# Performance work log

Hardware: AMD Instinct MI355X
Metric: run time of the kernel (lower is better)

The kernel has to match this reference:

```python
import jax, jax.numpy as jnp
import numpy as np

B, H, L, D = 2, 16, 2048, 64
EPS = 1e-6  # guard for all-zero causal rows after ReLU feature map


def setup_inputs() -> dict:
    key = jax.random.key(0)
    k1, k2, k3, k4, k5 = jax.random.split(key, 5)
    return {
        "query_states": jax.random.normal(k1, (B, H, L, D), dtype=jnp.float32),
        "key_states": jax.random.normal(k2, (B, H, L, D), dtype=jnp.float32),
        "value_states": jax.random.normal(k3, (B, H, L, D), dtype=jnp.float32),
        # LinearFeatureMap params: nn.Parameter(torch.rand(H, D, D)) -> uniform[0,1)
        "fm_query": jax.random.uniform(k4, (H, D, D), dtype=jnp.float32),
        "fm_key": jax.random.uniform(k5, (H, D, D), dtype=jnp.float32),
    }


def _feature_map(states, w):
    # states: [B,H,L,D]; w: [H,D,E]. Matches einsum('blhd,hde->blhe') after transposes.
    return jax.nn.relu(jnp.einsum('bhld,hde->bhle', states, w))


def reference(query_states, key_states, value_states, fm_query, fm_key):
    q = _feature_map(query_states, fm_query)   # [B,H,L,E]
    k = _feature_map(key_states, fm_key)       # [B,H,L,E]
    # quadratic (non-softmax) causal attention
    a = jnp.einsum('bhme,bhne->bhmn', q, k)    # [B,H,L,L]
    causal = jnp.tril(jnp.ones((L, L), dtype=bool))
    a = jnp.where(causal, a, 0.0)
    a = a / (jnp.sum(a, axis=-1, keepdims=True) + EPS)
    return jnp.einsum('bhmn,bhnd->bhmd', a, value_states)
```

## Files before the change

kernel.cpp:

```cpp
#include <hip/hip_runtime.h>
#include <hip/hip_bf16.h>

#define BH_  32
#define H_   16
#define L_   2048
#define D_   64
#define NC_  32
#define STR  72

typedef _Float16 half8  __attribute__((ext_vector_type(8)));
typedef float    floatx4 __attribute__((ext_vector_type(4)));

#define MFMA(a, b, c) __builtin_amdgcn_mfma_f32_16x16x32_f16((a), (b), (c), 0, 0, 0)

__device__ __forceinline__ half8 ldfrag(const _Float16* p, int row0, int k0) {
    const int lane = threadIdx.x & 63;
    const _Float16* q = p + (row0 + (lane & 15)) * STR + k0 + ((lane >> 4) << 3);
    return *(const half8*)q;
}

__global__ __launch_bounds__(256, 2)
void ka_chunksum(const float* __restrict__ K, const float* __restrict__ V,
                 const float* __restrict__ Wk,
                 float* __restrict__ Scs, float* __restrict__ zc) {
    __shared__ _Float16 sKin[64 * STR];
    __shared__ _Float16 sWT [64 * STR];
    __shared__ _Float16 sKT [64 * STR];
    __shared__ _Float16 sVT [64 * STR];

    const int c = blockIdx.x, bh = blockIdx.y, h = bh & (H_ - 1);
    const int tid = threadIdx.x, lane = tid & 63, w = tid >> 6;
    const int quad = lane >> 4, cl = lane & 15;

    const float* Kg = K + ((size_t)bh * L_ + c * 64) * D_;
    const float* Vg = V + ((size_t)bh * L_ + c * 64) * D_;
    const float* Wg = Wk + (size_t)h * 4096;

    for (int i = 0; i < 16; ++i) {
        int flat = i * 256 + tid;
        int r = flat >> 6, e = flat & 63;
        sKin[r * STR + e] = (_Float16)Kg[flat];
        sWT [e * STR + r] = (_Float16)Wg[flat];
        sVT [e * STR + r] = (_Float16)Vg[flat];
    }
    __syncthreads();

    half8 a0 = ldfrag(sKin, w * 16, 0), a1 = ldfrag(sKin, w * 16, 32);
    for (int et = 0; et < 4; ++et) {
        floatx4 acc = {0.f, 0.f, 0.f, 0.f};
        acc = MFMA(a0, ldfrag(sWT, et * 16, 0),  acc);
        acc = MFMA(a1, ldfrag(sWT, et * 16, 32), acc);
        #pragma unroll
        for (int r = 0; r < 4; ++r) {
            float v = acc[r] > 0.f ? acc[r] : 0.f;
            sKT[(et * 16 + cl) * STR + (w * 16 + quad * 4 + r)] = (_Float16)v;
        }
    }
    __syncthreads();

    if (tid < 64) {
        float s = 0.f;
        for (int n = 0; n < 64; ++n) s += (float)sKT[tid * STR + n];
        zc[((size_t)bh * NC_ + c) * 64 + tid] = s;
    }

    float* So = Scs + ((size_t)bh * NC_ + c) * 4096;
    half8 t0 = ldfrag(sKT, w * 16, 0), t1 = ldfrag(sKT, w * 16, 32);
    for (int et = 0; et < 4; ++et) {
        floatx4 acc = {0.f, 0.f, 0.f, 0.f};
        acc = MFMA(t0, ldfrag(sVT, et * 16, 0),  acc);
        acc = MFMA(t1, ldfrag(sVT, et * 16, 32), acc);
        #pragma unroll
        for (int r = 0; r < 4; ++r)
            So[(w * 16 + quad * 4 + r) * 64 + et * 16 + cl] = acc[r];
    }
}

__global__ __launch_bounds__(64)
void kp_prefix(float* __restrict__ Scs, float* __restrict__ zc) {
    const int bid = blockIdx.x, t = threadIdx.x;
    if (bid < BH_ * 64) {
        const int bh = bid >> 6, d = bid & 63;
        size_t base = (size_t)bh * NC_ * 4096 + (size_t)d * 64 + t;
        float run = 0.f;
        #pragma unroll
        for (int c = 0; c < NC_; ++c) {
            float v = Scs[base + (size_t)c * 4096];
            Scs[base + (size_t)c * 4096] = run;
            run += v;
        }
    } else {
        const int bh = bid - BH_ * 64;
        size_t base = (size_t)bh * NC_ * 64 + t;
        float run = 0.f;
        #pragma unroll
        for (int c = 0; c < NC_; ++c) {
            float v = zc[base + c * 64];
            zc[base + c * 64] = run;
            run += v;
        }
    }
}

__global__ __launch_bounds__(256, 2)
void kb_attn(const float* __restrict__ Q, const float* __restrict__ K,
             const float* __restrict__ V, const float* __restrict__ Wq,
             const float* __restrict__ Wk, const float* __restrict__ Sst,
             const float* __restrict__ zs, float* __restrict__ Out) {
    __shared__ _Float16 sQh[64 * STR];
    __shared__ _Float16 sQl[64 * STR];
    __shared__ _Float16 sWh[64 * STR];
    __shared__ _Float16 sWl[64 * STR];
    __shared__ _Float16 sVT[64 * STR];
    __shared__ _Float16 sST[64 * STR];
    __shared__ _Float16 sKB[64 * STR];
    __shared__ float sZ[64];
    __shared__ float sInv[64];

    const int c = blockIdx.x, bh = blockIdx.y, h = bh & (H_ - 1);
    const int tid = threadIdx.x, lane = tid & 63, w = tid >> 6;
    const int quad = lane >> 4, cl = lane & 15;

    const float* Qg = Q + ((size_t)bh * L_ + c * 64) * D_;
    const float* Kg = K + ((size_t)bh * L_ + c * 64) * D_;
    const float* Vg = V + ((size_t)bh * L_ + c * 64) * D_;
    const float* Wqg = Wq + (size_t)h * 4096;
    const float* Wkg = Wk + (size_t)h * 4096;
    const float* Sg = Sst + ((size_t)bh * NC_ + c) * 4096;
    const float* Zg = zs + ((size_t)bh * NC_ + c) * 64;

    for (int i = 0; i < 16; ++i) {
        int flat = i * 256 + tid;
        int r = flat >> 6, e = flat & 63;
        float q = Qg[flat];
        _Float16 qh = (_Float16)q;
        sQh[r * STR + e] = qh;
        sQl[r * STR + e] = (_Float16)(q - (float)qh);
        float wv = Wqg[flat];
        _Float16 wh = (_Float16)wv;
        sWh[e * STR + r] = wh;
        sWl[e * STR + r] = (_Float16)(wv - (float)wh);
        sKB[r * STR + e] = (_Float16)Kg[flat];
        sVT[e * STR + r] = (_Float16)Vg[flat];
        sST[e * STR + r] = (_Float16)Sg[flat];
    }
    if (tid < 64) sZ[tid] = Zg[tid];
    __syncthreads();

    half8 aqh0 = ldfrag(sQh, w * 16, 0), aqh1 = ldfrag(sQh, w * 16, 32);
    half8 aql0 = ldfrag(sQl, w * 16, 0), aql1 = ldfrag(sQl, w * 16, 32);
    float dq[4] = {0.f, 0.f, 0.f, 0.f};
    for (int et = 0; et < 4; ++et) {
        half8 bh0 = ldfrag(sWh, et * 16, 0), bh1 = ldfrag(sWh, et * 16, 32);
        half8 bl0 = ldfrag(sWl, et * 16, 0), bl1 = ldfrag(sWl, et * 16, 32);
        floatx4 acc = {0.f, 0.f, 0.f, 0.f};
        acc = MFMA(aqh0, bh0, acc);
        acc = MFMA(aqh1, bh1, acc);
        acc = MFMA(aqh0, bl0, acc);
        acc = MFMA(aqh1, bl1, acc);
        acc = MFMA(aql0, bh0, acc);
        acc = MFMA(aql1, bh1, acc);
        float zv = sZ[et * 16 + cl];
        #pragma unroll
        for (int r = 0; r < 4; ++r) {
            float v = acc[r] > 0.f ? acc[r] : 0.f;
            dq[r] += v * zv;
            _Float16 hi = (_Float16)v;
            sQh[(w * 16 + quad * 4 + r) * STR + et * 16 + cl] = hi;
            sQl[(w * 16 + quad * 4 + r) * STR + et * 16 + cl] = (_Float16)(v - (float)hi);
        }
    }
    #pragma unroll
    for (int r = 0; r < 4; ++r) {
        dq[r] += __shfl_xor(dq[r], 1);
        dq[r] += __shfl_xor(dq[r], 2);
        dq[r] += __shfl_xor(dq[r], 4);
        dq[r] += __shfl_xor(dq[r], 8);
    }
    __syncthreads();

    for (int i = 0; i < 16; ++i) {
        int flat = i * 256 + tid;
        int r = flat >> 6, e = flat & 63;
        sWh[e * STR + r] = (_Float16)Wkg[flat];
    }
    __syncthreads();

    half8 ak0 = ldfrag(sKB, w * 16, 0), ak1 = ldfrag(sKB, w * 16, 32);
    for (int et = 0; et < 4; ++et) {
        floatx4 acc = {0.f, 0.f, 0.f, 0.f};
        acc = MFMA(ak0, ldfrag(sWh, et * 16, 0),  acc);
        acc = MFMA(ak1, ldfrag(sWh, et * 16, 32), acc);
        #pragma unroll
        for (int r = 0; r < 4; ++r) {
            float v = acc[r] > 0.f ? acc[r] : 0.f;
            sKB[(w * 16 + quad * 4 + r) * STR + et * 16 + cl] = (_Float16)v;
        }
    }
    __syncthreads();

    half8 qh0 = ldfrag(sQh, w * 16, 0), qh1 = ldfrag(sQh, w * 16, 32);
    half8 ql0 = ldfrag(sQl, w * 16, 0), ql1 = ldfrag(sQl, w * 16, 32);
    _Float16* P = sWl;
    float rs[4] = {0.f, 0.f, 0.f, 0.f};
    for (int nt = 0; nt <= w; ++nt) {
        half8 b0 = ldfrag(sKB, nt * 16, 0), b1 = ldfrag(sKB, nt * 16, 32);
        floatx4 acc = {0.f, 0.f, 0.f, 0.f};
        acc = MFMA(qh0, b0, acc);
        acc = MFMA(qh1, b1, acc);
        acc = MFMA(ql0, b0, acc);
        acc = MFMA(ql1, b1, acc);
        #pragma unroll
        for (int r = 0; r < 4; ++r) {
            float v = acc[r];
            if (nt == w && cl > quad * 4 + r) v = 0.f;
            rs[r] += v;
            P[(w * 16 + quad * 4 + r) * STR + nt * 16 + cl] = (_Float16)v;
        }
    }
    for (int nt = w + 1; nt < 4; ++nt) {
        #pragma unroll
        for (int r = 0; r < 4; ++r)
            P[(w * 16 + quad * 4 + r) * STR + nt * 16 + cl] = (_Float16)0.f;
    }
    #pragma unroll
    for (int r = 0; r < 4; ++r) {
        float s = rs[r];
        s += __shfl_xor(s, 1);
        s += __shfl_xor(s, 2);
        s += __shfl_xor(s, 4);
        s += __shfl_xor(s, 8);
        if (cl == 0) sInv[w * 16 + quad * 4 + r] = 1.f / (s + dq[r] + 1e-6f);
    }
    __syncthreads();

    half8 p0 = ldfrag(P, w * 16, 0), p1 = ldfrag(P, w * 16, 32);
    float inv[4];
    #pragma unroll
    for (int r = 0; r < 4; ++r) inv[r] = sInv[w * 16 + quad * 4 + r];

    float* Og = Out + ((size_t)bh * L_ + c * 64) * D_;
    for (int et = 0; et < 4; ++et) {
        floatx4 acc = {0.f, 0.f, 0.f, 0.f};
        acc = MFMA(qh0, ldfrag(sST, et * 16, 0),  acc);
        acc = MFMA(qh1, ldfrag(sST, et * 16, 32), acc);
        acc = MFMA(ql0, ldfrag(sST, et * 16, 0),  acc);
        acc = MFMA(ql1, ldfrag(sST, et * 16, 32), acc);
        acc = MFMA(p0,  ldfrag(sVT, et * 16, 0),  acc);
        acc = MFMA(p1,  ldfrag(sVT, et * 16, 32), acc);
        #pragma unroll
        for (int r = 0; r < 4; ++r)
            Og[(w * 16 + quad * 4 + r) * 64 + et * 16 + cl] = acc[r] * inv[r];
    }
}

extern "C" void kernel_launch(void* const* d_in, const int* in_sizes, int n_in,
                              void* d_out, int out_size, void* d_ws, size_t ws_size,
                              hipStream_t stream) {
    const float* Q  = (const float*)d_in[0];
    const float* K  = (const float*)d_in[1];
    const float* V  = (const float*)d_in[2];
    const float* Wq = (const float*)d_in[3];
    const float* Wk = (const float*)d_in[4];
    float* Out = (float*)d_out;

    float* Scs = (float*)d_ws;
    float* zc  = Scs + (size_t)BH_ * NC_ * 4096;

    dim3 grid(NC_, BH_);
    hipLaunchKernelGGL(ka_chunksum, grid, dim3(256), 0, stream, K, V, Wk, Scs, zc);
    hipLaunchKernelGGL(kp_prefix, dim3(BH_ * 64 + BH_), dim3(64), 0, stream, Scs, zc);
    hipLaunchKernelGGL(kb_attn, grid, dim3(256), 0, stream, Q, K, V, Wq, Wk, Scs, zc, Out);
}
```

Measured before the change: 124.1 us.

## Precompute fp16 transposed weights and reuse key features across kernels

Adds a small kernel that transposes and converts the query and key feature-map weights to fp16 once per head, with hi/lo split for the query weights. The chunk-sum kernel now writes the ReLU key features and transposed V in fp16 to workspace, and the attention kernel reads them instead of recomputing the key feature map. Global loads are vectorized as float4/half8, and the row-normalizer is kept in registers rather than shared memory. This removes redundant key-projection work and scattered fp32 loads, at the cost of an extra launch and more workspace traffic. The Scs state matrix is now computed as V^T·K_f, so the attention kernel can read it untransposed.

Result: faster. 121.4 us (-2.2%).

```diff
diff --git a/kernel.cpp b/kernel.cpp
--- a/kernel.cpp
+++ b/kernel.cpp
@@ -8,7 +8,8 @@
 #define NC_  32
 #define STR  72
 
-typedef _Float16 half8  __attribute__((ext_vector_type(8)));
+typedef _Float16 half8 __attribute__((ext_vector_type(8)));
+typedef _Float16 half4 __attribute__((ext_vector_type(4)));
 typedef float    floatx4 __attribute__((ext_vector_type(4)));
 
 #define MFMA(a, b, c) __builtin_amdgcn_mfma_f32_16x16x32_f16((a), (b), (c), 0, 0, 0)
@@ -19,14 +20,48 @@
     return *(const half8*)q;
 }
 
+__global__ __launch_bounds__(256)
+void k0_weights(const float* __restrict__ Wq, const float* __restrict__ Wk,
+                _Float16* __restrict__ WqTh, _Float16* __restrict__ WqTl,
+                _Float16* __restrict__ WkT) {
+    __shared__ float sQ[64 * 65];
+    __shared__ float sK[64 * 65];
+    const int h = blockIdx.x, tid = threadIdx.x;
+    const float* Wqg = Wq + (size_t)h * 4096;
+    const float* Wkg = Wk + (size_t)h * 4096;
+    for (int i = 0; i < 16; ++i) {
+        int flat = i * 256 + tid;
+        int d = flat >> 6, e = flat & 63;
+        sQ[e * 65 + d] = Wqg[flat];
+        sK[e * 65 + d] = Wkg[flat];
+    }
+    __syncthreads();
+    for (int i = 0; i < 4; ++i) {
+        int flat = i * 1024 + tid * 4;
+        int e = flat >> 6, d0 = flat & 63;
+        half4 qh, ql, kh;
+        #pragma unroll
+        for (int j = 0; j < 4; ++j) {
+            float qv = sQ[e * 65 + d0 + j];
+            _Float16 hi = (_Float16)qv;
+            qh[j] = hi; ql[j] = (_Float16)(qv - (float)hi);
+            kh[j] = (_Float16)sK[e * 65 + d0 + j];
+        }
+        *(half4*)(WqTh + (size_t)h * 4096 + flat) = qh;
+        *(half4*)(WqTl + (size_t)h * 4096 + flat) = ql;
+        *(half4*)(WkT  + (size_t)h * 4096 + flat) = kh;
+    }
+}
+
 __global__ __launch_bounds__(256, 2)
 void ka_chunksum(const float* __restrict__ K, const float* __restrict__ V,
-                 const float* __restrict__ Wk,
-                 float* __restrict__ Scs, float* __restrict__ zc) {
-    __shared__ _Float16 sKin[64 * STR];
-    __shared__ _Float16 sWT [64 * STR];
-    __shared__ _Float16 sKT [64 * STR];
-    __shared__ _Float16 sVT [64 * STR];
+                 const _Float16* __restrict__ WkT,
+                 float* __restrict__ Scs, float* __restrict__ zc,
+                 _Float16* __restrict__ kf16, _Float16* __restrict__ VT16) {
+    __shared__ __align__(16) _Float16 sK  [64 * STR];
+    __shared__ __align__(16) _Float16 sWkT[64 * STR];
+    __shared__ __align__(16) _Float16 sVT [64 * STR];
+    __shared__ __align__(16) _Float16 sKfT[64 * STR];
 
     const int c = blockIdx.x, bh = blockIdx.y, h = bh & (H_ - 1);
     const int tid = threadIdx.x, lane = tid & 63, w = tid >> 6;
@@ -34,42 +69,66 @@
 
     const float* Kg = K + ((size_t)bh * L_ + c * 64) * D_;
     const float* Vg = V + ((size_t)bh * L_ + c * 64) * D_;
-    const float* Wg = Wk + (size_t)h * 4096;
-
-    for (int i = 0; i < 16; ++i) {
-        int flat = i * 256 + tid;
-        int r = flat >> 6, e = flat & 63;
-        sKin[r * STR + e] = (_Float16)Kg[flat];
-        sWT [e * STR + r] = (_Float16)Wg[flat];
-        sVT [e * STR + r] = (_Float16)Vg[flat];
-    }
-    __syncthreads();
-
-    half8 a0 = ldfrag(sKin, w * 16, 0), a1 = ldfrag(sKin, w * 16, 32);
+    const size_t cb = (size_t)bh * NC_ + c;
+
+    for (int i = 0; i < 4; ++i) {
+        int flat = i * 1024 + tid * 4;
+        int r = flat >> 6, e0 = flat & 63;
+        float4 kv = *(const float4*)(Kg + flat);
+        half4 kh = { (_Float16)kv.x, (_Float16)kv.y, (_Float16)kv.z, (_Float16)kv.w };
+        *(half4*)(sK + r * STR + e0) = kh;
+        float4 vv = *(const float4*)(Vg + flat);
+        sVT[(e0 + 0) * STR + r] = (_Float16)vv.x;
+        sVT[(e0 + 1) * STR + r] = (_Float16)vv.y;
+        sVT[(e0 + 2) * STR + r] = (_Float16)vv.z;
+        sVT[(e0 + 3) * STR + r] = (_Float16)vv.w;
+    }
+    for (int i = 0; i < 2; ++i) {
+        int flat = i * 2048 + tid * 8;
+        int e = flat >> 6, d0 = flat & 63;
+        *(half8*)(sWkT + e * STR + d0) = *(const half8*)(WkT + (size_t)h * 4096 + flat);
+    }
+    __syncthreads();
+
+    half8 ak0 = ldfrag(sK, w * 16, 0), ak1 = ldfrag(sK, w * 16, 32);
     for (int et = 0; et < 4; ++et) {
         floatx4 acc = {0.f, 0.f, 0.f, 0.f};
-        acc = MFMA(a0, ldfrag(sWT, et * 16, 0),  acc);
-        acc = MFMA(a1, ldfrag(sWT, et * 16, 32), acc);
+        acc = MFMA(ak0, ldfrag(sWkT, et * 16, 0),  acc);
+        acc = MFMA(ak1, ldfrag(sWkT, et * 16, 32), acc);
         #pragma unroll
         for (int r = 0; r < 4; ++r) {
             float v = acc[r] > 0.f ? acc[r] : 0.f;
-            sKT[(et * 16 + cl) * STR + (w * 16 + quad * 4 + r)] = (_Float16)v;
-        }
-    }
-    __syncthreads();
-
+            _Float16 hv = (_Float16)v;
+            int n = w * 16 + quad * 4 + r, f = et * 16 + cl;
+            sKfT[f * STR + n] = hv;
+            sK  [n * STR + f] = hv;
+        }
+    }
+    __syncthreads();
+
+    for (int i = 0; i < 2; ++i) {
+        int flat = i * 2048 + tid * 8;
+        int rr = flat >> 6, c0 = flat & 63;
+        *(half8*)(kf16 + cb * 4096 + flat) = *(const half8*)(sK  + rr * STR + c0);
+        *(half8*)(VT16 + cb * 4096 + flat) = *(const half8*)(sVT + rr * STR + c0);
+    }
     if (tid < 64) {
         float s = 0.f;
-        for (int n = 0; n < 64; ++n) s += (float)sKT[tid * STR + n];
-        zc[((size_t)bh * NC_ + c) * 64 + tid] = s;
-    }
-
-    float* So = Scs + ((size_t)bh * NC_ + c) * 4096;
-    half8 t0 = ldfrag(sKT, w * 16, 0), t1 = ldfrag(sKT, w * 16, 32);
+        #pragma unroll
+        for (int j = 0; j < 8; ++j) {
+            half8 hv = *(const half8*)(sKfT + tid * STR + j * 8);
+            #pragma unroll
+            for (int t = 0; t < 8; ++t) s += (float)hv[t];
+        }
+        zc[cb * 64 + tid] = s;
+    }
+
+    float* So = Scs + cb * 4096;
+    half8 av0 = ldfrag(sVT, w * 16, 0), av1 = ldfrag(sVT, w * 16, 32);
     for (int et = 0; et < 4; ++et) {
         floatx4 acc = {0.f, 0.f, 0.f, 0.f};
-        acc = MFMA(t0, ldfrag(sVT, et * 16, 0),  acc);
-        acc = MFMA(t1, ldfrag(sVT, et * 16, 32), acc);
+        acc = MFMA(av0, ldfrag(sKfT, et * 16, 0),  acc);
+        acc = MFMA(av1, ldfrag(sKfT, et * 16, 32), acc);
         #pragma unroll
         for (int r = 0; r < 4; ++r)
             So[(w * 16 + quad * 4 + r) * 64 + et * 16 + cl] = acc[r];
@@ -103,48 +162,53 @@
 }
 
 __global__ __launch_bounds__(256, 2)
-void kb_attn(const float* __restrict__ Q, const float* __restrict__ K,
-             const float* __restrict__ V, const float* __restrict__ Wq,
-             const float* __restrict__ Wk, const float* __restrict__ Sst,
+void kb_attn(const float* __restrict__ Q, const _Float16* __restrict__ WqTh,
+             const _Float16* __restrict__ WqTl, const _Float16* __restrict__ kf16,
+             const _Float16* __restrict__ VT16, const float* __restrict__ Sst,
              const float* __restrict__ zs, float* __restrict__ Out) {
-    __shared__ _Float16 sQh[64 * STR];
-    __shared__ _Float16 sQl[64 * STR];
-    __shared__ _Float16 sWh[64 * STR];
-    __shared__ _Float16 sWl[64 * STR];
-    __shared__ _Float16 sVT[64 * STR];
-    __shared__ _Float16 sST[64 * STR];
-    __shared__ _Float16 sKB[64 * STR];
+    __shared__ __align__(16) _Float16 sQh[64 * STR];
+    __shared__ __align__(16) _Float16 sQl[64 * STR];
+    __shared__ __align__(16) _Float16 sWh[64 * STR];
+    __shared__ __align__(16) _Float16 sWl[64 * STR];
+    __shared__ __align__(16) _Float16 sKf[64 * STR];
+    __shared__ __align__(16) _Float16 sVT[64 * STR];
+    __shared__ __align__(16) _Float16 sST[64 * STR];
     __shared__ float sZ[64];
-    __shared__ float sInv[64];
 
     const int c = blockIdx.x, bh = blockIdx.y, h = bh & (H_ - 1);
     const int tid = threadIdx.x, lane = tid & 63, w = tid >> 6;
     const int quad = lane >> 4, cl = lane & 15;
 
     const float* Qg = Q + ((size_t)bh * L_ + c * 64) * D_;
-    const float* Kg = K + ((size_t)bh * L_ + c * 64) * D_;
-    const float* Vg = V + ((size_t)bh * L_ + c * 64) * D_;
-    const float* Wqg = Wq + (size_t)h * 4096;
-    const float* Wkg = Wk + (size_t)h * 4096;
-    const float* Sg = Sst + ((size_t)bh * NC_ + c) * 4096;
-    const float* Zg = zs + ((size_t)bh * NC_ + c) * 64;
-
-    for (int i = 0; i < 16; ++i) {
-        int flat = i * 256 + tid;
-        int r = flat >> 6, e = flat & 63;
-        float q = Qg[flat];
-        _Float16 qh = (_Float16)q;
-        sQh[r * STR + e] = qh;
-        sQl[r * STR + e] = (_Float16)(q - (float)qh);
-        float wv = Wqg[flat];
-        _Float16 wh = (_Float16)wv;
-        sWh[e * STR + r] = wh;
-        sWl[e * STR + r] = (_Float16)(wv - (float)wh);
-        sKB[r * STR + e] = (_Float16)Kg[flat];
-        sVT[e * STR + r] = (_Float16)Vg[flat];
-        sST[e * STR + r] = (_Float16)Sg[flat];
-    }
-    if (tid < 64) sZ[tid] = Zg[tid];
+    const size_t cb = (size_t)bh * NC_ + c;
+    const float* Sg = Sst + cb * 4096;
+
+    for (int i = 0; i < 4; ++i) {
+        int flat = i * 1024 + tid * 4;
+        int r = flat >> 6, e0 = flat & 63;
+        float4 qv = *(const float4*)(Qg + flat);
+        half4 qh, ql;
+        #pragma unroll
+        for (int j = 0; j < 4; ++j) {
+            float x = (&qv.x)[j];
+            _Float16 hi = (_Float16)x;
+            qh[j] = hi; ql[j] = (_Float16)(x - (float)hi);
+        }
+        *(half4*)(sQh + r * STR + e0) = qh;
+        *(half4*)(sQl + r * STR + e0) = ql;
+        float4 sv = *(const float4*)(Sg + flat);
+        half4 sh = { (_Float16)sv.x, (_Float16)sv.y, (_Float16)sv.z, (_Float16)sv.w };
+        *(half4*)(sST + r * STR + e0) = sh;
+    }
+    for (int i = 0; i < 2; ++i) {
+        int flat = i * 2048 + tid * 8;
+        int rr = flat >> 6, c0 = flat & 63;
+        *(half8*)(sWh + rr * STR + c0) = *(const half8*)(WqTh + (size_t)h * 4096 + flat);
+        *(half8*)(sWl + rr * STR + c0) = *(const half8*)(WqTl + (size_t)h * 4096 + flat);
+        *(half8*)(sKf + rr * STR + c0) = *(const half8*)(kf16 + cb * 4096 + flat);
+        *(half8*)(sVT + rr * STR + c0) = *(const half8*)(VT16 + cb * 4096 + flat);
+    }
+    if (tid < 64) sZ[tid] = zs[cb * 64 + tid];
     __syncthreads();
 
     half8 aqh0 = ldfrag(sQh, w * 16, 0), aqh1 = ldfrag(sQh, w * 16, 32);
@@ -166,8 +230,9 @@
             float v = acc[r] > 0.f ? acc[r] : 0.f;
             dq[r] += v * zv;
             _Float16 hi = (_Float16)v;
-            sQh[(w * 16 + quad * 4 + r) * STR + et * 16 + cl] = hi;
-            sQl[(w * 16 + quad * 4 + r) * STR + et * 16 + cl] = (_Float16)(v - (float)hi);
+            int row = w * 16 + quad * 4 + r, col = et * 16 + cl;
+            sQh[row * STR + col] = hi;
+            sQl[row * STR + col] = (_Float16)(v - (float)hi);
         }
     }
     #pragma unroll
@@ -179,32 +244,13 @@
     }
     __syncthreads();
 
-    for (int i = 0; i < 16; ++i) {
-        int flat = i * 256 + tid;
-        int r = flat >> 6, e = flat & 63;
-        sWh[e * STR + r] = (_Float16)Wkg[flat];
-    }
-    __syncthreads();
-
-    half8 ak0 = ldfrag(sKB, w * 16, 0), ak1 = ldfrag(sKB, w * 16, 32);
-    for (int et = 0; et < 4; ++et) {
-        floatx4 acc = {0.f, 0.f, 0.f, 0.f};
-        acc = MFMA(ak0, ldfrag(sWh, et * 16, 0),  acc);
-        acc = MFMA(ak1, ldfrag(sWh, et * 16, 32), acc);
-        #pragma unroll
-        for (int r = 0; r < 4; ++r) {
-            float v = acc[r] > 0.f ? acc[r] : 0.f;
-            sKB[(w * 16 + quad * 4 + r) * STR + et * 16 + cl] = (_Float16)v;
-        }
-    }
-    __syncthreads();
-
     half8 qh0 = ldfrag(sQh, w * 16, 0), qh1 = ldfrag(sQh, w * 16, 32);
     half8 ql0 = ldfrag(sQl, w * 16, 0), ql1 = ldfrag(sQl, w * 16, 32);
     _Float16* P = sWl;
     float rs[4] = {0.f, 0.f, 0.f, 0.f};
+    float inv[4];
     for (int nt = 0; nt <= w; ++nt) {
-        half8 b0 = ldfrag(sKB, nt * 16, 0), b1 = ldfrag(sKB, nt * 16, 32);
+        half8 b0 = ldfrag(sKf, nt * 16, 0), b1 = ldfrag(sKf, nt * 16, 32);
         floatx4 acc = {0.f, 0.f, 0.f, 0.f};
         acc = MFMA(qh0, b0, acc);
         acc = MFMA(qh1, b1, acc);
@@ -230,24 +276,21 @@
         s += __shfl_xor(s, 2);
         s += __shfl_xor(s, 4);
         s += __shfl_xor(s, 8);
-        if (cl == 0) sInv[w * 16 + quad * 4 + r] = 1.f / (s + dq[r] + 1e-6f);
+        inv[r] = 1.f / (s + dq[r] + 1e-6f);
     }
     __syncthreads();
 
     half8 p0 = ldfrag(P, w * 16, 0), p1 = ldfrag(P, w * 16, 32);
-    float inv[4];
-    #pragma unroll
-    for (int r = 0; r < 4; ++r) inv[r] = sInv[w * 16 + quad * 4 + r];
-
     float* Og = Out + ((size_t)bh * L_ + c * 64) * D_;
     for (int et = 0; et < 4; ++et) {
         floatx4 acc = {0.f, 0.f, 0.f, 0.f};
-        acc = MFMA(qh0, ldfrag(sST, et * 16, 0),  acc);
-        acc = MFMA(qh1, ldfrag(sST, et * 16, 32), acc);
-        acc = MFMA(ql0, ldfrag(sST, et * 16, 0),  acc);
-        acc = MFMA(ql1, ldfrag(sST, et * 16, 32), acc);
-        acc = MFMA(p0,  ldfrag(sVT, et * 16, 0),  acc);
-        acc = MFMA(p1,  ldfrag(sVT, et * 16, 32), acc);
+        half8 s0 = ldfrag(sST, et * 16, 0), s1 = ldfrag(sST, et * 16, 32);
+        acc = MFMA(qh0, s0, acc);
+        acc = MFMA(qh1, s1, acc);
+        acc = MFMA(ql0, s0, acc);
+        acc = MFMA(ql1, s1, acc);
+        acc = MFMA(p0, ldfrag(sVT, et * 16, 0),  acc);
+        acc = MFMA(p1, ldfrag(sVT, et * 16, 32), acc);
         #pragma unroll
         for (int r = 0; r < 4; ++r)
             Og[(w * 16 + quad * 4 + r) * 64 + et * 16 + cl] = acc[r] * inv[r];
@@ -264,11 +307,17 @@
     const float* Wk = (const float*)d_in[4];
     float* Out = (float*)d_out;
 
-    float* Scs = (float*)d_ws;
-    float* zc  = Scs + (size_t)BH_ * NC_ * 4096;
+    float*    Scs  = (float*)d_ws;
+    float*    zc   = Scs + (size_t)BH_ * NC_ * 4096;
+    _Float16* kf16 = (_Float16*)(zc + (size_t)BH_ * NC_ * 64);
+    _Float16* VT16 = kf16 + (size_t)BH_ * NC_ * 4096;
+    _Float16* WqTh = VT16 + (size_t)BH_ * NC_ * 4096;
+    _Float16* WqTl = WqTh + (size_t)H_ * 4096;
+    _Float16* WkT  = WqTl + (size_t)H_ * 4096;
 
     dim3 grid(NC_, BH_);
-    hipLaunchKernelGGL(ka_chunksum, grid, dim3(256), 0, stream, K, V, Wk, Scs, zc);
+    hipLaunchKernelGGL(k0_weights, dim3(H_), dim3(256), 0, stream, Wq, Wk, WqTh, WqTl, WkT);
+    hipLaunchKernelGGL(ka_chunksum, grid, dim3(256), 0, stream, K, V, WkT, Scs, zc, kf16, VT16);
     hipLaunchKernelGGL(kp_prefix, dim3(BH_ * 64 + BH_), dim3(64), 0, stream, Scs, zc);
-    hipLaunchKernelGGL(kb_attn, grid, dim3(256), 0, stream, Q, K, V, Wq, Wk, Scs, zc, Out);
-}
+    hipLaunchKernelGGL(kb_attn, grid, dim3(256), 0, stream, Q, WqTh, WqTl, kf16, VT16, Scs, zc, Out);
+}
```
